# Optimization experiments

Measured on AMD Instinct MI355X. Metric: run time of the kernel, lower is better.

Reference implementation:

```python
import jax, jax.numpy as jnp
import numpy as np

CODEBOOK_SIZE = 1024
COMMITMENT_COST = 0.25
ENTROPY_RATIO = 0.1
ENTROPY_TEMP = 0.01


def squared_euclidean_distance(a, b):
    # a: [N, D], b: [K, D] -> [N, K]
    a2 = jnp.sum(a * a, axis=1, keepdims=True)            # [N, 1]
    b2 = jnp.sum(b * b, axis=1)[None, :]                  # [1, K]
    return a2 + b2 - 2.0 * (a @ b.T)


def entropy_loss(affinity, temperature):
    # MaskGIT-style 'softmax' entropy loss
    flat = affinity.reshape(-1, affinity.shape[-1]) / temperature
    probs = jax.nn.softmax(flat, axis=-1)
    log_probs = jax.nn.log_softmax(flat + 1e-5, axis=-1)
    target_probs = probs
    avg_probs = jnp.mean(target_probs, axis=0)
    avg_entropy = -jnp.sum(avg_probs * jnp.log(avg_probs + 1e-5))
    sample_entropy = -jnp.mean(jnp.sum(target_probs * log_probs, axis=-1))
    return sample_entropy - avg_entropy


def setup_inputs() -> dict:
    key = jax.random.key(0)
    kx, kc = jax.random.split(key)
    d = 256
    x = jax.random.normal(kx, (32, 32, 32, 256), dtype=jnp.float32)
    # variance_scaling(scale=1.0, mode='fan_in', distribution='uniform') for
    # shape (K, D): fan_in = D, limit = sqrt(3 * scale / fan_in)
    lim = float(np.sqrt(3.0 / d))
    codebook = jax.random.uniform(kc, (CODEBOOK_SIZE, d), jnp.float32, -lim, lim)
    return {"x": x, "codebook": codebook}


def reference(x, codebook):
    flat = x.reshape(-1, x.shape[-1])                      # [N, D]
    dist = squared_euclidean_distance(flat, codebook)      # [N, K]
    encoding_indices = jnp.argmin(dist, axis=-1)           # [N]
    # one_hot @ codebook == gather of codebook rows (same math, no one-hot)
    quantized = jnp.take(codebook, encoding_indices, axis=0).reshape(x.shape)

    e_latent_loss = jnp.mean((jax.lax.stop_gradient(quantized) - x) ** 2) * COMMITMENT_COST
    q_latent_loss = jnp.mean((quantized - jax.lax.stop_gradient(x)) ** 2)
    ent_loss = entropy_loss(-dist, ENTROPY_TEMP) * ENTROPY_RATIO
    loss = (e_latent_loss + q_latent_loss + ent_loss).astype(jnp.float32)

    # straight-through estimator
    quantized_st = x + jax.lax.stop_gradient(quantized - x)
    return quantized_st, loss, encoding_indices.reshape(x.shape[:-1])
```

## Files before the change

### kernel.cpp

```cpp
#include <hip/hip_runtime.h>
#include <math.h>
#include <float.h>

#define D 256
#define K 1024
#define NROWS 32768
#define MARGIN 1.0f
#define MAXCAND 12

#define LOSS_OFF 8388608
#define IDX_OFF  8388609

typedef _Float16 h8 __attribute__((ext_vector_type(8)));
typedef float    v4f __attribute__((ext_vector_type(4)));
typedef const __attribute__((address_space(1))) unsigned int* gas_u32p;
typedef __attribute__((address_space(3))) unsigned int* las_u32p;

__device__ __forceinline__ float np_sq_block128(const float* a) {
    float r0 = __fmul_rn(a[0], a[0]);
    float r1 = __fmul_rn(a[1], a[1]);
    float r2 = __fmul_rn(a[2], a[2]);
    float r3 = __fmul_rn(a[3], a[3]);
    float r4 = __fmul_rn(a[4], a[4]);
    float r5 = __fmul_rn(a[5], a[5]);
    float r6 = __fmul_rn(a[6], a[6]);
    float r7 = __fmul_rn(a[7], a[7]);
    for (int i = 8; i < 128; i += 8) {
        r0 = __fadd_rn(r0, __fmul_rn(a[i + 0], a[i + 0]));
        r1 = __fadd_rn(r1, __fmul_rn(a[i + 1], a[i + 1]));
        r2 = __fadd_rn(r2, __fmul_rn(a[i + 2], a[i + 2]));
        r3 = __fadd_rn(r3, __fmul_rn(a[i + 3], a[i + 3]));
        r4 = __fadd_rn(r4, __fmul_rn(a[i + 4], a[i + 4]));
        r5 = __fadd_rn(r5, __fmul_rn(a[i + 5], a[i + 5]));
        r6 = __fadd_rn(r6, __fmul_rn(a[i + 6], a[i + 6]));
        r7 = __fadd_rn(r7, __fmul_rn(a[i + 7], a[i + 7]));
    }
    float tA = __fadd_rn(__fadd_rn(r0, r1), __fadd_rn(r2, r3));
    float tB = __fadd_rn(__fadd_rn(r4, r5), __fadd_rn(r6, r7));
    return __fadd_rn(tA, tB);
}

__global__ void vq_prep(const float* __restrict__ cb, float* __restrict__ b2,
                        h8* __restrict__ cfrag, float* __restrict__ avg_acc,
                        float* __restrict__ scal) {
    int tid = blockIdx.x * 256 + threadIdx.x;
    {
        int ln = tid & 15;
        int qd = (tid >> 4) & 3;
        int T  = (tid >> 6) & 63;
        int s  = tid >> 12;
        int k  = T * 16 + ln;
        const float* c = cb + (size_t)k * D + s * 32 + qd * 8;
        float4 v0 = *(const float4*)c;
        float4 v1 = *(const float4*)(c + 4);
        h8 f;
        f[0] = (_Float16)v0.x; f[1] = (_Float16)v0.y;
        f[2] = (_Float16)v0.z; f[3] = (_Float16)v0.w;
        f[4] = (_Float16)v1.x; f[5] = (_Float16)v1.y;
        f[6] = (_Float16)v1.z; f[7] = (_Float16)v1.w;
        cfrag[tid] = f;
    }
    if (tid < K) {
        const float* c = cb + (size_t)tid * D;
        b2[tid] = __fadd_rn(np_sq_block128(c), np_sq_block128(c + 128));
    }
    if (tid >= 1024 && tid < 2048) avg_acc[tid - 1024] = 0.f;
    if (tid >= 2048 && tid < 2050) scal[tid - 2048] = 0.f;
}

__global__ __launch_bounds__(256, 2)
void vq_mfma(const float* __restrict__ x, const float* __restrict__ cb,
             const h8* __restrict__ cfrag, const float* __restrict__ b2,
             float* __restrict__ avg_acc, float* __restrict__ scal,
             float* __restrict__ out)
{
    __shared__ __align__(16) h8 bbuf[4096];
    __shared__ float mred[4][32];
    __shared__ int   kred[4][32];
    __shared__ float sred[4][32];
    __shared__ float tred[4][32];
    __shared__ int   bkl[32];
    __shared__ int   candn[32];
    __shared__ int   candk[32][MAXCAND];
    __shared__ __align__(16) float xbuf[256];

    const int t   = threadIdx.x;
    const int w   = t >> 6;
    const int q   = w;
    const int l64 = t & 63;
    const int qd  = l64 >> 4;
    const int ln  = l64 & 15;
    const int r0  = blockIdx.x * 32;

    if (t < 32) candn[t] = 0;

    v4f acc[2][16];
    #pragma unroll
    for (int rt = 0; rt < 2; ++rt)
        #pragma unroll
        for (int tt = 0; tt < 16; ++tt) acc[rt][tt] = (v4f)0.f;

    const float* ab[2] = { x + (size_t)(r0 + ln) * D,
                           x + (size_t)(r0 + 16 + ln) * D };

    float4 pa[4];
    #pragma unroll
    for (int rt = 0; rt < 2; ++rt) {
        pa[2 * rt]     = *(const float4*)(ab[rt] + qd * 8);
        pa[2 * rt + 1] = *(const float4*)(ab[rt] + qd * 8 + 4);
    }

    for (int s = 0; s < 8; ++s) {
        #pragma unroll
        for (int kk = 0; kk < 16; ++kk) {
            int T = w * 16 + kk;
            const h8* gsrc = cfrag + ((size_t)(s * 64 + T)) * 64 + l64;
            __builtin_amdgcn_global_load_lds(
                (gas_u32p)(const void*)gsrc,
                (las_u32p)(void*)(bbuf + T * 64),
                16, 0, 0);
        }
        asm volatile("s_waitcnt vmcnt(0)" ::: "memory");

        h8 af[2];
        #pragma unroll
        for (int rt = 0; rt < 2; ++rt) {
            float4 a0 = pa[2 * rt], a1 = pa[2 * rt + 1];
            af[rt][0] = (_Float16)a0.x; af[rt][1] = (_Float16)a0.y;
            af[rt][2] = (_Float16)a0.z; af[rt][3] = (_Float16)a0.w;
            af[rt][4] = (_Float16)a1.x; af[rt][5] = (_Float16)a1.y;
            af[rt][6] = (_Float16)a1.z; af[rt][7] = (_Float16)a1.w;
        }
        if (s < 7) {
            #pragma unroll
            for (int rt = 0; rt < 2; ++rt) {
                pa[2 * rt]     = *(const float4*)(ab[rt] + (s + 1) * 32 + qd * 8);
                pa[2 * rt + 1] = *(const float4*)(ab[rt] + (s + 1) * 32 + qd * 8 + 4);
            }
        }
        #pragma unroll
        for (int tt = 0; tt < 16; ++tt) {
            h8 bf = bbuf[(16 * q + tt) * 64 + l64];
            acc[0][tt] = __builtin_amdgcn_mfma_f32_16x16x32_f16(af[0], bf, acc[0][tt], 0, 0, 0);
            acc[1][tt] = __builtin_amdgcn_mfma_f32_16x16x32_f16(af[1], bf, acc[1][tt], 0, 0, 0);
        }
    }

    float b2c[16];
    #pragma unroll
    for (int tt = 0; tt < 16; ++tt) b2c[tt] = b2[256 * q + 16 * tt + ln];
    #pragma unroll
    for (int rt = 0; rt < 2; ++rt)
        #pragma unroll
        for (int tt = 0; tt < 16; ++tt)
            #pragma unroll
            for (int r = 0; r < 4; ++r)
                acc[rt][tt][r] = 200.f * acc[rt][tt][r] - 100.f * b2c[tt];

    float m[2][4]; int bk[2][4];
    #pragma unroll
    for (int rt = 0; rt < 2; ++rt)
        #pragma unroll
        for (int r = 0; r < 4; ++r) { m[rt][r] = -INFINITY; bk[rt][r] = K; }
    #pragma unroll
    for (int tt = 0; tt < 16; ++tt)
        #pragma unroll
        for (int rt = 0; rt < 2; ++rt)
            #pragma unroll
            for (int r = 0; r < 4; ++r) {
                float z = acc[rt][tt][r];
                int code = 256 * q + 16 * tt + ln;
                if (z > m[rt][r]) { m[rt][r] = z; bk[rt][r] = code; }
            }
    #pragma unroll
    for (int off = 1; off < 16; off <<= 1)
        #pragma unroll
        for (int rt = 0; rt < 2; ++rt)
            #pragma unroll
            for (int r = 0; r < 4; ++r) {
                float om = __shfl_xor(m[rt][r], off);
                int   ok = __shfl_xor(bk[rt][r], off);
                if (om > m[rt][r] || (om == m[rt][r] && ok < bk[rt][r])) {
                    m[rt][r] = om; bk[rt][r] = ok;
                }
            }
    if (ln == 0)
        #pragma unroll
        for (int rt = 0; rt < 2; ++rt)
            #pragma unroll
            for (int r = 0; r < 4; ++r) {
                int rl = 16 * rt + 4 * qd + r;
                mred[q][rl] = m[rt][r]; kred[q][rl] = bk[rt][r];
            }
    __syncthreads();

    float mf[2][4]; int kf[2][4];
    #pragma unroll
    for (int rt = 0; rt < 2; ++rt)
        #pragma unroll
        for (int r = 0; r < 4; ++r) {
            int rl = 16 * rt + 4 * qd + r;
            mf[rt][r] = mred[0][rl]; kf[rt][r] = kred[0][rl];
            #pragma unroll
            for (int qq = 1; qq < 4; ++qq) {
                float mm = mred[qq][rl];
                if (mm > mf[rt][r]) { mf[rt][r] = mm; kf[rt][r] = kred[qq][rl]; }
            }
        }

    float S[2][4] = {{0,0,0,0},{0,0,0,0}}, T[2][4] = {{0,0,0,0},{0,0,0,0}};
    #pragma unroll
    for (int tt = 0; tt < 16; ++tt)
        #pragma unroll
        for (int rt = 0; rt < 2; ++rt)
            #pragma unroll
            for (int r = 0; r < 4; ++r) {
                float z  = acc[rt][tt][r];
                float zz = z - mf[rt][r];
                float e  = __expf(zz);
                if (z > mf[rt][r] - MARGIN) {
                    int rl = 16 * rt + 4 * qd + r;
                    int slot = atomicAdd(&candn[rl], 1);
                    if (slot < MAXCAND) candk[rl][slot] = 256 * q + 16 * tt + ln;
                }
                S[rt][r] += e; T[rt][r] += zz * e;
                acc[rt][tt][r] = e;
            }
    #pragma unroll
    for (int off = 1; off < 16; off <<= 1)
        #pragma unroll
        for (int rt = 0; rt < 2; ++rt)
            #pragma unroll
            for (int r = 0; r < 4; ++r) {
                S[rt][r] += __shfl_xor(S[rt][r], off);
                T[rt][r] += __shfl_xor(T[rt][r], off);
            }
    if (ln == 0)
        #pragma unroll
        for (int rt = 0; rt < 2; ++rt)
            #pragma unroll
            for (int r = 0; r < 4; ++r) {
                int rl = 16 * rt + 4 * qd + r;
                sred[q][rl] = S[rt][r]; tred[q][rl] = T[rt][r];
            }
    __syncthreads();

    float iS[2][4];
    float hsum = 0.f;
    #pragma unroll
    for (int rt = 0; rt < 2; ++rt)
        #pragma unroll
        for (int r = 0; r < 4; ++r) {
            int rl = 16 * rt + 4 * qd + r;
            float Sf = sred[0][rl] + sred[1][rl] + sred[2][rl] + sred[3][rl];
            float Tf = tred[0][rl] + tred[1][rl] + tred[2][rl] + tred[3][rl];
            iS[rt][r] = 1.f / Sf;
            if (q == 0 && ln == 0) {
                bkl[rl] = kf[rt][r];
                hsum += Tf * iS[rt][r] - __logf(Sf);
            }
        }
    if (q == 0 && ln == 0) atomicAdd(&scal[1], hsum);

    #pragma unroll
    for (int tt = 0; tt < 16; ++tt)
        #pragma unroll
        for (int rt = 0; rt < 2; ++rt)
            #pragma unroll
            for (int r = 0; r < 4; ++r) {
                float p = acc[rt][tt][r] * iS[rt][r];
                if (p > 1e-12f)
                    atomicAdd(&avg_acc[256 * q + 16 * tt + ln], p);
            }
    __syncthreads();

    if (w == 0) {
        for (int row = 0; row < 32; ++row) {
            int tc = candn[row];
            if (tc < 2) continue;
            if (tc > MAXCAND) tc = MAXCAND;
            const float* xr = x + (size_t)(r0 + row) * D;
            *(float4*)&xbuf[l64 * 4] = *(const float4*)(xr + l64 * 4);
            float a2f = __fadd_rn(np_sq_block128(xbuf), np_sq_block128(xbuf + 128));
            float bestd = FLT_MAX; int bestk = K;
            for (int c = 0; c < tc; ++c) {
                int k = candk[row][c];
                double sdot = 0.0;
                #pragma unroll
                for (int dd = 0; dd < 4; ++dd)
                    sdot += (double)cb[(size_t)k * D + l64 * 4 + dd] *
                            (double)xbuf[l64 * 4 + dd];
                #pragma unroll
                for (int off = 32; off > 0; off >>= 1)
                    sdot += __shfl_xor(sdot, off);
                float abf = (float)sdot;
                float dnp = __fsub_rn(__fadd_rn(a2f, b2[k]), __fmul_rn(2.0f, abf));
                if (dnp < bestd || (dnp == bestd && k < bestk)) {
                    bestd = dnp; bestk = k;
                }
            }
            if (l64 == 0) bkl[row] = bestk;
        }
    }
    __syncthreads();

    float wmse = 0.f;
    #pragma unroll
    for (int rr = 0; rr < 8; ++rr) {
        int rl  = 8 * w + rr;
        int row = r0 + rl;
        int bk2 = bkl[rl];
        float4 xv = *(const float4*)(x  + (size_t)row * D + l64 * 4);
        float4 qv = *(const float4*)(cb + (size_t)bk2 * D + l64 * 4);
        float dx = qv.x - xv.x, dy = qv.y - xv.y, dz = qv.z - xv.z, dw = qv.w - xv.w;
        float4 st;
        st.x = xv.x + dx; st.y = xv.y + dy; st.z = xv.z + dz; st.w = xv.w + dw;
        *(float4*)(out + (size_t)row * D + l64 * 4) = st;
        if (l64 == 0) out[IDX_OFF + row] = (float)bk2;
        wmse += dx * dx + dy * dy + dz * dz + dw * dw;
    }
    #pragma unroll
    for (int off = 32; off > 0; off >>= 1)
        wmse += __shfl_xor(wmse, off);
    if (l64 == 0) atomicAdd(&scal[0], wmse);
}

__global__ __launch_bounds__(1024)
void vq_fin(const float* __restrict__ avg_acc, const float* __restrict__ scal,
            float* __restrict__ out)
{
    __shared__ float sred[16];
    int t = threadIdx.x;
    float ap = avg_acc[t] * (1.f / 32768.f);
    float v = ap * logf(ap + 1e-5f);
    #pragma unroll
    for (int off = 32; off > 0; off >>= 1) v += __shfl_xor(v, off);
    if ((t & 63) == 0) sred[t >> 6] = v;
    __syncthreads();
    if (t == 0) {
        float s = 0.f;
        for (int w = 0; w < 16; ++w) s += sred[w];
        float avg_entropy = -s;
        float sampleH = -scal[1] * (1.f / 32768.f);
        float mse = scal[0] * (1.f / 8388608.f);
        float loss = 1.25f * mse + 0.1f * (sampleH - avg_entropy);
        out[LOSS_OFF] = loss;
    }
}

extern "C" void kernel_launch(void* const* d_in, const int* in_sizes, int n_in,
                              void* d_out, int out_size, void* d_ws, size_t ws_size,
                              hipStream_t stream)
{
    const float* x  = (const float*)d_in[0];
    const float* cb = (const float*)d_in[1];
    float* out = (float*)d_out;
    float* ws  = (float*)d_ws;
    float* b2      = ws;
    float* avg_acc = ws + K;
    float* scal    = ws + 2 * K;
    h8*    cfrag   = (h8*)((char*)d_ws + 16384);

    vq_prep<<<128, 256, 0, stream>>>(cb, b2, cfrag, avg_acc, scal);
    vq_mfma<<<NROWS / 32, 256, 0, stream>>>(x, cb, cfrag, b2, avg_acc, scal, out);
    vq_fin<<<1, 1024, 0, stream>>>(avg_acc, scal, out);
}
```

Before: 200.5 us.

## Double-buffer codebook fragments in registers, use 512-thread blocks, fuse final reduction

The main kernel moves to 512 threads (8 waves), each owning 128 codes. Codebook fragments are read straight from global memory into double-buffered registers instead of staged through LDS with a full vmcnt wait, and all x fragments are preconverted to fp16 up front. The finalize kernel is folded into the main kernel with a last-block-done counter, b2 precompute is parallelised across lanes with shuffles, and one launch is removed. Register pressure rises from holding all A fragments, and every wave now loads B separately from L2 rather than sharing an LDS copy.

```diff
diff --git a/kernel.cpp b/kernel.cpp
--- a/kernel.cpp
+++ b/kernel.cpp
@@ -5,6 +5,7 @@
 #define D 256
 #define K 1024
 #define NROWS 32768
+#define NBLK (NROWS / 32)
 #define MARGIN 1.0f
 #define MAXCAND 12
 
@@ -13,8 +14,6 @@
 
 typedef _Float16 h8 __attribute__((ext_vector_type(8)));
 typedef float    v4f __attribute__((ext_vector_type(4)));
-typedef const __attribute__((address_space(1))) unsigned int* gas_u32p;
-typedef __attribute__((address_space(3))) unsigned int* las_u32p;
 
 __device__ __forceinline__ float np_sq_block128(const float* a) {
     float r0 = __fmul_rn(a[0], a[0]);
@@ -60,29 +59,43 @@
         f[6] = (_Float16)v1.z; f[7] = (_Float16)v1.w;
         cfrag[tid] = f;
     }
-    if (tid < K) {
-        const float* c = cb + (size_t)tid * D;
-        b2[tid] = __fadd_rn(np_sq_block128(c), np_sq_block128(c + 128));
+    int gw = tid >> 6;
+    if (gw < 256) {
+        int l    = tid & 63;
+        int code = gw * 4 + (l >> 4);
+        int j    = l & 7;
+        int half = (l >> 3) & 1;
+        const float* c = cb + (size_t)code * D + half * 128 + j;
+        float v = __fmul_rn(c[0], c[0]);
+        #pragma unroll
+        for (int m = 1; m < 16; ++m)
+            v = __fadd_rn(v, __fmul_rn(c[8 * m], c[8 * m]));
+        v = __fadd_rn(v, __shfl_xor(v, 1));
+        v = __fadd_rn(v, __shfl_xor(v, 2));
+        v = __fadd_rn(v, __shfl_xor(v, 4));
+        v = __fadd_rn(v, __shfl_xor(v, 8));
+        if ((l & 15) == 0) b2[code] = v;
     }
     if (tid >= 1024 && tid < 2048) avg_acc[tid - 1024] = 0.f;
-    if (tid >= 2048 && tid < 2050) scal[tid - 2048] = 0.f;
+    if (tid >= 2048 && tid < 2051) scal[tid - 2048] = 0.f;
 }
 
-__global__ __launch_bounds__(256, 2)
+__global__ __launch_bounds__(512, 2)
 void vq_mfma(const float* __restrict__ x, const float* __restrict__ cb,
              const h8* __restrict__ cfrag, const float* __restrict__ b2,
              float* __restrict__ avg_acc, float* __restrict__ scal,
              float* __restrict__ out)
 {
-    __shared__ __align__(16) h8 bbuf[4096];
-    __shared__ float mred[4][32];
-    __shared__ int   kred[4][32];
-    __shared__ float sred[4][32];
-    __shared__ float tred[4][32];
+    __shared__ float mred[8][32];
+    __shared__ int   kred[8][32];
+    __shared__ float sred[8][32];
+    __shared__ float tred[8][32];
     __shared__ int   bkl[32];
     __shared__ int   candn[32];
     __shared__ int   candk[32][MAXCAND];
     __shared__ __align__(16) float xbuf[256];
+    __shared__ int   lastflag;
+    __shared__ float finred[8];
 
     const int t   = threadIdx.x;
     const int w   = t >> 6;
@@ -94,65 +107,55 @@
 
     if (t < 32) candn[t] = 0;
 
-    v4f acc[2][16];
-    #pragma unroll
-    for (int rt = 0; rt < 2; ++rt)
-        #pragma unroll
-        for (int tt = 0; tt < 16; ++tt) acc[rt][tt] = (v4f)0.f;
-
-    const float* ab[2] = { x + (size_t)(r0 + ln) * D,
-                           x + (size_t)(r0 + 16 + ln) * D };
-
-    float4 pa[4];
-    #pragma unroll
-    for (int rt = 0; rt < 2; ++rt) {
-        pa[2 * rt]     = *(const float4*)(ab[rt] + qd * 8);
-        pa[2 * rt + 1] = *(const float4*)(ab[rt] + qd * 8 + 4);
-    }
-
+    h8 afr[2][8];
+    #pragma unroll
+    for (int m = 0; m < 2; ++m) {
+        const float* xr = x + (size_t)(r0 + 16 * m + ln) * D + qd * 8;
+        #pragma unroll
+        for (int s = 0; s < 8; ++s) {
+            float4 a0 = *(const float4*)(xr + 32 * s);
+            float4 a1 = *(const float4*)(xr + 32 * s + 4);
+            h8 f;
+            f[0] = (_Float16)a0.x; f[1] = (_Float16)a0.y;
+            f[2] = (_Float16)a0.z; f[3] = (_Float16)a0.w;
+            f[4] = (_Float16)a1.x; f[5] = (_Float16)a1.y;
+            f[6] = (_Float16)a1.z; f[7] = (_Float16)a1.w;
+            afr[m][s] = f;
+        }
+    }
+
+    v4f acc[2][8];
+    #pragma unroll
+    for (int rt = 0; rt < 2; ++rt)
+        #pragma unroll
+        for (int tt = 0; tt < 8; ++tt) acc[rt][tt] = (v4f)0.f;
+
+    const h8* bp = cfrag + (size_t)(8 * w) * 64 + l64;
+    h8 bb[2][8];
+    #pragma unroll
+    for (int tt = 0; tt < 8; ++tt) bb[0][tt] = bp[tt * 64];
+    #pragma unroll
     for (int s = 0; s < 8; ++s) {
-        #pragma unroll
-        for (int kk = 0; kk < 16; ++kk) {
-            int T = w * 16 + kk;
-            const h8* gsrc = cfrag + ((size_t)(s * 64 + T)) * 64 + l64;
-            __builtin_amdgcn_global_load_lds(
-                (gas_u32p)(const void*)gsrc,
-                (las_u32p)(void*)(bbuf + T * 64),
-                16, 0, 0);
-        }
-        asm volatile("s_waitcnt vmcnt(0)" ::: "memory");
-
-        h8 af[2];
-        #pragma unroll
-        for (int rt = 0; rt < 2; ++rt) {
-            float4 a0 = pa[2 * rt], a1 = pa[2 * rt + 1];
-            af[rt][0] = (_Float16)a0.x; af[rt][1] = (_Float16)a0.y;
-            af[rt][2] = (_Float16)a0.z; af[rt][3] = (_Float16)a0.w;
-            af[rt][4] = (_Float16)a1.x; af[rt][5] = (_Float16)a1.y;
-            af[rt][6] = (_Float16)a1.z; af[rt][7] = (_Float16)a1.w;
-        }
+        const int cur = s & 1, nxt = cur ^ 1;
         if (s < 7) {
             #pragma unroll
-            for (int rt = 0; rt < 2; ++rt) {
-                pa[2 * rt]     = *(const float4*)(ab[rt] + (s + 1) * 32 + qd * 8);
-                pa[2 * rt + 1] = *(const float4*)(ab[rt] + (s + 1) * 32 + qd * 8 + 4);
-            }
-        }
-        #pragma unroll
-        for (int tt = 0; tt < 16; ++tt) {
-            h8 bf = bbuf[(16 * q + tt) * 64 + l64];
-            acc[0][tt] = __builtin_amdgcn_mfma_f32_16x16x32_f16(af[0], bf, acc[0][tt], 0, 0, 0);
-            acc[1][tt] = __builtin_amdgcn_mfma_f32_16x16x32_f16(af[1], bf, acc[1][tt], 0, 0, 0);
-        }
-    }
-
-    float b2c[16];
-    #pragma unroll
-    for (int tt = 0; tt < 16; ++tt) b2c[tt] = b2[256 * q + 16 * tt + ln];
-    #pragma unroll
-    for (int rt = 0; rt < 2; ++rt)
-        #pragma unroll
-        for (int tt = 0; tt < 16; ++tt)
+            for (int tt = 0; tt < 8; ++tt)
+                bb[nxt][tt] = bp[(s + 1) * 4096 + tt * 64];
+        }
+        #pragma unroll
+        for (int tt = 0; tt < 8; ++tt) {
+            acc[0][tt] = __builtin_amdgcn_mfma_f32_16x16x32_f16(afr[0][s], bb[cur][tt], acc[0][tt], 0, 0, 0);
+            acc[1][tt] = __builtin_amdgcn_mfma_f32_16x16x32_f16(afr[1][s], bb[cur][tt], acc[1][tt], 0, 0, 0);
+        }
+    }
+
+    float b2c[8];
+    #pragma unroll
+    for (int tt = 0; tt < 8; ++tt) b2c[tt] = b2[128 * q + 16 * tt + ln];
+    #pragma unroll
+    for (int rt = 0; rt < 2; ++rt)
+        #pragma unroll
+        for (int tt = 0; tt < 8; ++tt)
             #pragma unroll
             for (int r = 0; r < 4; ++r)
                 acc[rt][tt][r] = 200.f * acc[rt][tt][r] - 100.f * b2c[tt];
@@ -163,13 +166,13 @@
         #pragma unroll
         for (int r = 0; r < 4; ++r) { m[rt][r] = -INFINITY; bk[rt][r] = K; }
     #pragma unroll
-    for (int tt = 0; tt < 16; ++tt)
+    for (int tt = 0; tt < 8; ++tt)
         #pragma unroll
         for (int rt = 0; rt < 2; ++rt)
             #pragma unroll
             for (int r = 0; r < 4; ++r) {
                 float z = acc[rt][tt][r];
-                int code = 256 * q + 16 * tt + ln;
+                int code = 128 * q + 16 * tt + ln;
                 if (z > m[rt][r]) { m[rt][r] = z; bk[rt][r] = code; }
             }
     #pragma unroll
@@ -202,7 +205,7 @@
             int rl = 16 * rt + 4 * qd + r;
             mf[rt][r] = mred[0][rl]; kf[rt][r] = kred[0][rl];
             #pragma unroll
-            for (int qq = 1; qq < 4; ++qq) {
+            for (int qq = 1; qq < 8; ++qq) {
                 float mm = mred[qq][rl];
                 if (mm > mf[rt][r]) { mf[rt][r] = mm; kf[rt][r] = kred[qq][rl]; }
             }
@@ -210,7 +213,7 @@
 
     float S[2][4] = {{0,0,0,0},{0,0,0,0}}, T[2][4] = {{0,0,0,0},{0,0,0,0}};
     #pragma unroll
-    for (int tt = 0; tt < 16; ++tt)
+    for (int tt = 0; tt < 8; ++tt)
         #pragma unroll
         for (int rt = 0; rt < 2; ++rt)
             #pragma unroll
@@ -221,7 +224,7 @@
                 if (z > mf[rt][r] - MARGIN) {
                     int rl = 16 * rt + 4 * qd + r;
                     int slot = atomicAdd(&candn[rl], 1);
-                    if (slot < MAXCAND) candk[rl][slot] = 256 * q + 16 * tt + ln;
+                    if (slot < MAXCAND) candk[rl][slot] = 128 * q + 16 * tt + ln;
                 }
                 S[rt][r] += e; T[rt][r] += zz * e;
                 acc[rt][tt][r] = e;
@@ -252,8 +255,9 @@
         #pragma unroll
         for (int r = 0; r < 4; ++r) {
             int rl = 16 * rt + 4 * qd + r;
-            float Sf = sred[0][rl] + sred[1][rl] + sred[2][rl] + sred[3][rl];
-            float Tf = tred[0][rl] + tred[1][rl] + tred[2][rl] + tred[3][rl];
+            float Sf = 0.f, Tf = 0.f;
+            #pragma unroll
+            for (int qq = 0; qq < 8; ++qq) { Sf += sred[qq][rl]; Tf += tred[qq][rl]; }
             iS[rt][r] = 1.f / Sf;
             if (q == 0 && ln == 0) {
                 bkl[rl] = kf[rt][r];
@@ -263,14 +267,14 @@
     if (q == 0 && ln == 0) atomicAdd(&scal[1], hsum);
 
     #pragma unroll
-    for (int tt = 0; tt < 16; ++tt)
+    for (int tt = 0; tt < 8; ++tt)
         #pragma unroll
         for (int rt = 0; rt < 2; ++rt)
             #pragma unroll
             for (int r = 0; r < 4; ++r) {
                 float p = acc[rt][tt][r] * iS[rt][r];
                 if (p > 1e-12f)
-                    atomicAdd(&avg_acc[256 * q + 16 * tt + ln], p);
+                    atomicAdd(&avg_acc[128 * q + 16 * tt + ln], p);
             }
     __syncthreads();
 
@@ -306,8 +310,8 @@
 
     float wmse = 0.f;
     #pragma unroll
-    for (int rr = 0; rr < 8; ++rr) {
-        int rl  = 8 * w + rr;
+    for (int rr = 0; rr < 4; ++rr) {
+        int rl  = 4 * w + rr;
         int row = r0 + rl;
         int bk2 = bkl[rl];
         float4 xv = *(const float4*)(x  + (size_t)row * D + l64 * 4);
@@ -323,28 +327,33 @@
     for (int off = 32; off > 0; off >>= 1)
         wmse += __shfl_xor(wmse, off);
     if (l64 == 0) atomicAdd(&scal[0], wmse);
-}
-
-__global__ __launch_bounds__(1024)
-void vq_fin(const float* __restrict__ avg_acc, const float* __restrict__ scal,
-            float* __restrict__ out)
-{
-    __shared__ float sred[16];
-    int t = threadIdx.x;
-    float ap = avg_acc[t] * (1.f / 32768.f);
-    float v = ap * logf(ap + 1e-5f);
-    #pragma unroll
-    for (int off = 32; off > 0; off >>= 1) v += __shfl_xor(v, off);
-    if ((t & 63) == 0) sred[t >> 6] = v;
+
     __syncthreads();
     if (t == 0) {
-        float s = 0.f;
-        for (int w = 0; w < 16; ++w) s += sred[w];
-        float avg_entropy = -s;
-        float sampleH = -scal[1] * (1.f / 32768.f);
-        float mse = scal[0] * (1.f / 8388608.f);
-        float loss = 1.25f * mse + 0.1f * (sampleH - avg_entropy);
-        out[LOSS_OFF] = loss;
+        unsigned prev = atomicAdd((unsigned*)(scal + 2), 1u);
+        lastflag = (prev == NBLK - 1) ? 1 : 0;
+    }
+    __syncthreads();
+    if (lastflag) {
+        float v = 0.f;
+        #pragma unroll
+        for (int h = 0; h < 2; ++h) {
+            int i = t + 512 * h;
+            float ap = atomicAdd(&avg_acc[i], 0.0f) * (1.f / 32768.f);
+            v += ap * logf(ap + 1e-5f);
+        }
+        #pragma unroll
+        for (int off = 32; off > 0; off >>= 1) v += __shfl_xor(v, off);
+        if (l64 == 0) finred[w] = v;
+        __syncthreads();
+        if (t == 0) {
+            float s = 0.f;
+            for (int ww = 0; ww < 8; ++ww) s += finred[ww];
+            float avg_entropy = -s;
+            float sampleH = -atomicAdd(&scal[1], 0.0f) * (1.f / 32768.f);
+            float mse = atomicAdd(&scal[0], 0.0f) * (1.f / 8388608.f);
+            out[LOSS_OFF] = 1.25f * mse + 0.1f * (sampleH - avg_entropy);
+        }
     }
 }
 
@@ -362,6 +371,5 @@
     h8*    cfrag   = (h8*)((char*)d_ws + 16384);
 
     vq_prep<<<128, 256, 0, stream>>>(cb, b2, cfrag, avg_acc, scal);
-    vq_mfma<<<NROWS / 32, 256, 0, stream>>>(x, cb, cfrag, b2, avg_acc, scal, out);
-    vq_fin<<<1, 1024, 0, stream>>>(avg_acc, scal, out);
+    vq_mfma<<<NBLK, 512, 0, stream>>>(x, cb, cfrag, b2, avg_acc, scal, out);
 }
```

After: 249.8 us. +24.6%, slower.
